# Optimization experiments

Measured on AMD Instinct MI355X. Metric: run time of the kernel, lower is better.

The kernel has to match this reference:

```python
import jax, jax.numpy as jnp
import numpy as np
from jax import lax

B, N = 4096, 512          # batch, sequence length (input_dim = 2*N)
H1, H2 = 64, 256          # hidden sizes of the two stacked LSTMs
E = 20                    # embed dim
OUT = 2


def _lstm_step(x, h, c, Wih, Whh, b):
    # gates in PyTorch order: i, f, g, o
    g = x @ Wih.T + h @ Whh.T + b
    i, f, gg, o = jnp.split(g, 4, axis=-1)
    c_new = jax.nn.sigmoid(f) * c + jax.nn.sigmoid(i) * jnp.tanh(gg)
    h_new = jax.nn.sigmoid(o) * jnp.tanh(c_new)
    return h_new, c_new


def setup_inputs() -> dict:
    key = jax.random.key(0)
    ks = jax.random.split(key, 9)
    s = lambda fan_in: 1.0 / np.sqrt(fan_in)
    return {
        "x": jax.random.normal(ks[0], (B, 2 * N), dtype=jnp.float32),
        "W_embed": jax.random.uniform(ks[1], (E, 2), minval=-s(2), maxval=s(2), dtype=jnp.float32),
        "Wih1": jax.random.uniform(ks[2], (4 * H1, E), minval=-s(H1), maxval=s(H1), dtype=jnp.float32),
        "Whh1": jax.random.uniform(ks[3], (4 * H1, H1), minval=-s(H1), maxval=s(H1), dtype=jnp.float32),
        "b1": jax.random.uniform(ks[4], (4 * H1,), minval=-s(H1), maxval=s(H1), dtype=jnp.float32),
        "Wih2": jax.random.uniform(ks[5], (4 * H2, H1), minval=-s(H2), maxval=s(H2), dtype=jnp.float32),
        "Whh2": jax.random.uniform(ks[6], (4 * H2, H2), minval=-s(H2), maxval=s(H2), dtype=jnp.float32),
        "b2": jax.random.uniform(ks[7], (4 * H2,), minval=-s(H2), maxval=s(H2), dtype=jnp.float32),
        "Wout": jax.random.uniform(ks[8], (OUT, H2), minval=-s(H2), maxval=s(H2), dtype=jnp.float32),
        "bout": jnp.zeros((OUT,), dtype=jnp.float32),
    }


def reference(x, W_embed, Wih1, Whh1, b1, Wih2, Whh2, b2, Wout, bout):
    b = x.shape[0]
    tokens = x.reshape(b, -1, 2).transpose(1, 0, 2)         # (n, b, 2)
    embedded = jax.nn.relu(tokens @ W_embed.T)              # (n, b, 20)

    def step(carry, xt):
        h, c = carry
        h, c = _lstm_step(xt, h, c, Wih1, Whh1, b1)
        return (h, c), None

    h0 = jnp.zeros((b, H1), dtype=x.dtype)
    (h64, _), _ = lax.scan(step, (h0, h0), embedded)        # last hidden (b, 64)

    # second LSTM applied to the 2-D last-hidden as a single timestep
    hz = jnp.zeros((b, H2), dtype=x.dtype)
    h256, _ = _lstm_step(h64, hz, hz, Wih2, Whh2, b2)       # (b, 256)

    return h256 @ Wout.T + bout                             # (b, 2)
```

## Files before the change

kernel.cpp:

```cpp
#include <hip/hip_runtime.h>

typedef _Float16 f16x8 __attribute__((ext_vector_type(8)));
typedef float    f32x4 __attribute__((ext_vector_type(4)));

#define NSTEP 512
#define CHUNK 8
#define NCHUNK (NSTEP / CHUNK)
#define LOG2E     1.4426950408889634f
#define TWOLOG2E  2.8853900817779268f

__device__ __forceinline__ float exp2_(float v) { return __builtin_amdgcn_exp2f(v); }

__device__ __forceinline__ float lstm_act_(float gi, float gf, float gg, float go, float& c) {
    float eg = exp2_(gg);
    float ei = exp2_(gi);
    float ef = exp2_(gf);
    float eo = exp2_(go);
    float X  = (eg + 1.0f) * (1.0f + ei);
    float Y  = 1.0f + ef;
    float r  = __builtin_amdgcn_rcpf(X * Y);
    c = fmaf(r * X, c, (eg - 1.0f) * (r * Y));
    float ec = exp2_(fminf(c * TWOLOG2E, 30.0f));
    float r2 = __builtin_amdgcn_rcpf((ec + 1.0f) * (1.0f + eo));
    return (ec - 1.0f) * r2;
}
__device__ __forceinline__ float sig_(float v) {
    return __builtin_amdgcn_rcpf(1.0f + exp2_(-v * LOG2E));
}
__device__ __forceinline__ float tanh_(float v) {
    return 1.0f - 2.0f * __builtin_amdgcn_rcpf(exp2_(v * TWOLOG2E) + 1.0f);
}

__device__ __forceinline__ void bar_() {
    asm volatile("s_waitcnt lgkmcnt(0)" ::: "memory");
    __builtin_amdgcn_s_barrier();
    asm volatile("" ::: "memory");
}

__global__ __launch_bounds__(512, 2) void lstm_mfma16_kernel(
    const float* __restrict__ x,     const float* __restrict__ Wemb,
    const float* __restrict__ Wih1,  const float* __restrict__ Whh1,
    const float* __restrict__ b1,    const float* __restrict__ Wih2,
    const float* __restrict__ b2,    const float* __restrict__ Wout,
    const float* __restrict__ bout,  float* __restrict__ out)
{
    __shared__ __align__(16) _Float16 P[2][2][4][16][8];
    __shared__ __align__(16) _Float16 Pe[2][CHUNK][4][16][8];
    __shared__ __align__(16) float h2tmp[16 * 64];
    __shared__ __align__(16) float h2s[256 * 16];
    __shared__ float part[32 * 16 * 2];

    const int t   = threadIdx.x;
    const int l   = t & 63;
    const int w   = t >> 6;
    const int m   = l & 15;
    const int q   = l >> 4;
    const int b0  = blockIdx.x * 16;

    f16x8 whh[2][2], whE[2];
    f32x4 bias4[2];
    #pragma unroll
    for (int tt = 0; tt < 2; ++tt) {
        const int tau = 2 * w + tt;
        const int g = m & 3;
        const float sc = (g == 2) ? TWOLOG2E : -LOG2E;
        const int n = g * 64 + 4 * tau + (m >> 2);
        #pragma unroll
        for (int c = 0; c < 2; ++c)
            #pragma unroll
            for (int jj = 0; jj < 8; ++jj)
                whh[tt][c][jj] = (_Float16)(Whh1[n * 64 + c * 32 + (q << 3) + jj] * sc);
        #pragma unroll
        for (int jj = 0; jj < 8; ++jj) {
            int k = (q << 3) + jj;
            whE[tt][jj] = (_Float16)((k < 20) ? Wih1[n * 20 + k] * sc : 0.0f);
        }
        #pragma unroll
        for (int r = 0; r < 4; ++r) {
            float scr = (r == 2) ? TWOLOG2E : -LOG2E;
            bias4[tt][r] = b1[r * 64 + 4 * tau + q] * scr;
        }
    }

    const int myuA = 8 * w + q;
    const int myuB = 8 * w + 4 + q;
    _Float16* hwA = &P[0][myuA >> 5][(myuA >> 3) & 3][m][myuA & 7];
    _Float16* hwB = &P[0][myuB >> 5][(myuB >> 3) & 3][m][myuB & 7];
    const _Float16* rb = &P[0][0][q][m][0];

    const float* xp[5]; _Float16* pe[5];
    float we0[5], we1[5];
    float2 xv[5];
    #pragma unroll
    for (int k = 0; k < 5; ++k) {
        int v  = t + 512 * k;
        int d  = v % 20, pr = v / 20;
        int bb = pr & 15, s = pr >> 4;
        we0[k] = Wemb[2 * d];
        we1[k] = Wemb[2 * d + 1];
        pe[k]  = &Pe[0][s][d >> 3][bb][d & 7];
        xp[k]  = x + (size_t)(b0 + bb) * (2 * NSTEP) + 2 * s;
        xv[k]  = *(const float2*)xp[k];
    }

    ((_Float16*)P)[t]       = (_Float16)0.0f;
    ((_Float16*)P)[t + 512] = (_Float16)0.0f;
    {
        _Float16* pz = (_Float16*)Pe;
        #pragma unroll
        for (int k = 0; k < 16; ++k) pz[t + 512 * k] = (_Float16)0.0f;
    }
    __syncthreads();
    #pragma unroll
    for (int k = 0; k < 5; ++k)
        pe[k][0] = (_Float16)fmaxf(fmaf(xv[k].x, we0[k], xv[k].y * we1[k]), 0.0f);
    #pragma unroll
    for (int k = 0; k < 5; ++k) { xp[k] += 16; xv[k] = *(const float2*)xp[k]; }
    __syncthreads();

    float cA = 0.0f, cB = 0.0f;
    for (int ch = 0; ch < NCHUNK; ++ch) {
        const int pb = ch & 1;
        const _Float16* peR = (const _Float16*)Pe + pb * 4096;

        f32x4 axA[CHUNK], axB[CHUNK];
        #pragma unroll
        for (int j = 0; j < CHUNK; ++j) {
            f16x8 fe = *(const f16x8*)(peR + j * 512 + q * 128 + m * 8);
            axA[j] = __builtin_amdgcn_mfma_f32_16x16x32_f16(whE[0], fe, bias4[0], 0, 0, 0);
            axB[j] = __builtin_amdgcn_mfma_f32_16x16x32_f16(whE[1], fe, bias4[1], 0, 0, 0);
        }

        #pragma unroll
        for (int j = 0; j < CHUNK; ++j) {
            const int pr = j & 1;
            f16x8 f0 = *(const f16x8*)(rb + pr * 1024);
            f16x8 f1 = *(const f16x8*)(rb + pr * 1024 + 512);
            f32x4 aA = __builtin_amdgcn_mfma_f32_16x16x32_f16(whh[0][0], f0, axA[j], 0, 0, 0);
            f32x4 aB = __builtin_amdgcn_mfma_f32_16x16x32_f16(whh[1][0], f0, axB[j], 0, 0, 0);
            aA = __builtin_amdgcn_mfma_f32_16x16x32_f16(whh[0][1], f1, aA, 0, 0, 0);
            aB = __builtin_amdgcn_mfma_f32_16x16x32_f16(whh[1][1], f1, aB, 0, 0, 0);
            float hA = lstm_act_(aA[0], aA[1], aA[2], aA[3], cA);
            float hB = lstm_act_(aB[0], aB[1], aB[2], aB[3], cB);
            hwA[(pr ^ 1) * 1024] = (_Float16)hA;
            hwB[(pr ^ 1) * 1024] = (_Float16)hB;
            if (j == 0) {
                #pragma unroll
                for (int k = 0; k < 5; ++k)
                    pe[k][(pb ^ 1) * 4096] =
                        (_Float16)fmaxf(fmaf(xv[k].x, we0[k], xv[k].y * we1[k]), 0.0f);
                if (ch + 2 < NCHUNK) {
                    #pragma unroll
                    for (int k = 0; k < 5; ++k) { xp[k] += 16; xv[k] = *(const float2*)xp[k]; }
                }
            }
            bar_();
        }
    }

    #pragma unroll
    for (int r = 0; r < 2; ++r) {
        int tt = t + 512 * r;
        int b = tt >> 6, k = tt & 63;
        h2tmp[tt] = (float)P[0][k >> 5][(k >> 3) & 3][b][k & 7];
    }
    __syncthreads();

    {
        const int u = t & 255;
        const int bh0 = (t >> 8) * 8;
        float acci[8], accg[8], acco[8];
        float bi2 = b2[u], bg2 = b2[512 + u], bo2 = b2[768 + u];
        #pragma unroll
        for (int b = 0; b < 8; ++b) { acci[b] = bi2; accg[b] = bg2; acco[b] = bo2; }
        for (int k4 = 0; k4 < 64; k4 += 4) {
            float4 wi = *(const float4*)&Wih2[(size_t)u * 64 + k4];
            float4 wg = *(const float4*)&Wih2[(size_t)(512 + u) * 64 + k4];
            float4 wo = *(const float4*)&Wih2[(size_t)(768 + u) * 64 + k4];
            #pragma unroll
            for (int b = 0; b < 8; ++b) {
                float4 hb = *(const float4*)&h2tmp[(bh0 + b) * 64 + k4];
                acci[b] += wi.x * hb.x + wi.y * hb.y + wi.z * hb.z + wi.w * hb.w;
                accg[b] += wg.x * hb.x + wg.y * hb.y + wg.z * hb.z + wg.w * hb.w;
                acco[b] += wo.x * hb.x + wo.y * hb.y + wo.z * hb.z + wo.w * hb.w;
            }
        }
        #pragma unroll
        for (int b = 0; b < 8; ++b) {
            float c2 = sig_(acci[b]) * tanh_(accg[b]);
            h2s[u * 16 + bh0 + b] = sig_(acco[b]) * tanh_(c2);
        }
    }
    __syncthreads();

    {
        int b = t & 15, grp = t >> 4;
        float p0 = 0.f, p1 = 0.f;
        #pragma unroll
        for (int uu = grp * 8; uu < grp * 8 + 8; ++uu) {
            float hvv = h2s[uu * 16 + b];
            p0 += hvv * Wout[uu];
            p1 += hvv * Wout[256 + uu];
        }
        part[(grp * 16 + b) * 2 + 0] = p0;
        part[(grp * 16 + b) * 2 + 1] = p1;
    }
    __syncthreads();
    if (t < 32) {
        int b = t >> 1, o = t & 1;
        float s0 = bout[o];
        for (int grp = 0; grp < 32; ++grp) s0 += part[(grp * 16 + b) * 2 + o];
        out[(size_t)(b0 + b) * 2 + o] = s0;
    }
}

extern "C" void kernel_launch(void* const* d_in, const int* in_sizes, int n_in,
                              void* d_out, int out_size, void* d_ws, size_t ws_size,
                              hipStream_t stream) {
    const float* x    = (const float*)d_in[0];
    const float* Wemb = (const float*)d_in[1];
    const float* Wih1 = (const float*)d_in[2];
    const float* Whh1 = (const float*)d_in[3];
    const float* b1   = (const float*)d_in[4];
    const float* Wih2 = (const float*)d_in[5];
    const float* b2   = (const float*)d_in[7];
    const float* Wout = (const float*)d_in[8];
    const float* bout = (const float*)d_in[9];
    float* out = (float*)d_out;

    lstm_mfma16_kernel<<<256, 512, 0, stream>>>(
        x, Wemb, Wih1, Whh1, b1, Wih2, b2, Wout, bout, out);
}
```

Before: 291.7 us.

## Halve block to four waves, each computing four gate tiles per step

Shrinks the workgroup from 512 to 256 threads. Each wave now owns four 16-unit gate tiles of the recurrent LSTM instead of two. The embedding chunk drops from 8 to 4 steps, and the second-LSTM and output tail are remapped to 16 batches per thread. The aim is to make the per-timestep barrier cheaper by syncing fewer waves and to give each wave more independent MFMA chains for ILP. The cost is one wave per SIMD, which leaves less cross-wave latency hiding, plus more registers per wave.

```diff
diff --git a/kernel.cpp b/kernel.cpp
--- a/kernel.cpp
+++ b/kernel.cpp
@@ -4,7 +4,7 @@
 typedef float    f32x4 __attribute__((ext_vector_type(4)));
 
 #define NSTEP 512
-#define CHUNK 8
+#define CHUNK 4
 #define NCHUNK (NSTEP / CHUNK)
 #define LOG2E     1.4426950408889634f
 #define TWOLOG2E  2.8853900817779268f
@@ -37,7 +37,7 @@
     asm volatile("" ::: "memory");
 }
 
-__global__ __launch_bounds__(512, 2) void lstm_mfma16_kernel(
+__global__ __launch_bounds__(256, 1) void lstm_mfma16_kernel(
     const float* __restrict__ x,     const float* __restrict__ Wemb,
     const float* __restrict__ Wih1,  const float* __restrict__ Whh1,
     const float* __restrict__ b1,    const float* __restrict__ Wih2,
@@ -48,7 +48,7 @@
     __shared__ __align__(16) _Float16 Pe[2][CHUNK][4][16][8];
     __shared__ __align__(16) float h2tmp[16 * 64];
     __shared__ __align__(16) float h2s[256 * 16];
-    __shared__ float part[32 * 16 * 2];
+    __shared__ float part[16 * 16 * 2];
 
     const int t   = threadIdx.x;
     const int l   = t & 63;
@@ -57,11 +57,11 @@
     const int q   = l >> 4;
     const int b0  = blockIdx.x * 16;
 
-    f16x8 whh[2][2], whE[2];
-    f32x4 bias4[2];
-    #pragma unroll
-    for (int tt = 0; tt < 2; ++tt) {
-        const int tau = 2 * w + tt;
+    f16x8 whh[4][2], whE[4];
+    f32x4 bias4[4];
+    #pragma unroll
+    for (int tt = 0; tt < 4; ++tt) {
+        const int tau = 4 * w + tt;
         const int g = m & 3;
         const float sc = (g == 2) ? TWOLOG2E : -LOG2E;
         const int n = g * 64 + 4 * tau + (m >> 2);
@@ -82,10 +82,12 @@
         }
     }
 
-    const int myuA = 8 * w + q;
-    const int myuB = 8 * w + 4 + q;
-    _Float16* hwA = &P[0][myuA >> 5][(myuA >> 3) & 3][m][myuA & 7];
-    _Float16* hwB = &P[0][myuB >> 5][(myuB >> 3) & 3][m][myuB & 7];
+    _Float16* hw[4];
+    #pragma unroll
+    for (int tt = 0; tt < 4; ++tt) {
+        const int myu = 16 * w + 4 * tt + q;
+        hw[tt] = &P[0][myu >> 5][(myu >> 3) & 3][m][myu & 7];
+    }
     const _Float16* rb = &P[0][0][q][m][0];
 
     const float* xp[5]; _Float16* pe[5];
@@ -93,7 +95,7 @@
     float2 xv[5];
     #pragma unroll
     for (int k = 0; k < 5; ++k) {
-        int v  = t + 512 * k;
+        int v  = t + 256 * k;
         int d  = v % 20, pr = v / 20;
         int bb = pr & 15, s = pr >> 4;
         we0[k] = Wemb[2 * d];
@@ -103,32 +105,33 @@
         xv[k]  = *(const float2*)xp[k];
     }
 
-    ((_Float16*)P)[t]       = (_Float16)0.0f;
-    ((_Float16*)P)[t + 512] = (_Float16)0.0f;
+    #pragma unroll
+    for (int k = 0; k < 8; ++k) ((_Float16*)P)[t + 256 * k] = (_Float16)0.0f;
     {
         _Float16* pz = (_Float16*)Pe;
         #pragma unroll
-        for (int k = 0; k < 16; ++k) pz[t + 512 * k] = (_Float16)0.0f;
+        for (int k = 0; k < 16; ++k) pz[t + 256 * k] = (_Float16)0.0f;
     }
     __syncthreads();
     #pragma unroll
     for (int k = 0; k < 5; ++k)
         pe[k][0] = (_Float16)fmaxf(fmaf(xv[k].x, we0[k], xv[k].y * we1[k]), 0.0f);
     #pragma unroll
-    for (int k = 0; k < 5; ++k) { xp[k] += 16; xv[k] = *(const float2*)xp[k]; }
-    __syncthreads();
-
-    float cA = 0.0f, cB = 0.0f;
+    for (int k = 0; k < 5; ++k) { xp[k] += 2 * CHUNK; xv[k] = *(const float2*)xp[k]; }
+    __syncthreads();
+
+    float cst[4] = {0.f, 0.f, 0.f, 0.f};
     for (int ch = 0; ch < NCHUNK; ++ch) {
         const int pb = ch & 1;
-        const _Float16* peR = (const _Float16*)Pe + pb * 4096;
-
-        f32x4 axA[CHUNK], axB[CHUNK];
+        const _Float16* peR = (const _Float16*)Pe + pb * 2048;
+
+        f32x4 ax[4][CHUNK];
         #pragma unroll
         for (int j = 0; j < CHUNK; ++j) {
             f16x8 fe = *(const f16x8*)(peR + j * 512 + q * 128 + m * 8);
-            axA[j] = __builtin_amdgcn_mfma_f32_16x16x32_f16(whE[0], fe, bias4[0], 0, 0, 0);
-            axB[j] = __builtin_amdgcn_mfma_f32_16x16x32_f16(whE[1], fe, bias4[1], 0, 0, 0);
+            #pragma unroll
+            for (int tt = 0; tt < 4; ++tt)
+                ax[tt][j] = __builtin_amdgcn_mfma_f32_16x16x32_f16(whE[tt], fe, bias4[tt], 0, 0, 0);
         }
 
         #pragma unroll
@@ -136,22 +139,26 @@
             const int pr = j & 1;
             f16x8 f0 = *(const f16x8*)(rb + pr * 1024);
             f16x8 f1 = *(const f16x8*)(rb + pr * 1024 + 512);
-            f32x4 aA = __builtin_amdgcn_mfma_f32_16x16x32_f16(whh[0][0], f0, axA[j], 0, 0, 0);
-            f32x4 aB = __builtin_amdgcn_mfma_f32_16x16x32_f16(whh[1][0], f0, axB[j], 0, 0, 0);
-            aA = __builtin_amdgcn_mfma_f32_16x16x32_f16(whh[0][1], f1, aA, 0, 0, 0);
-            aB = __builtin_amdgcn_mfma_f32_16x16x32_f16(whh[1][1], f1, aB, 0, 0, 0);
-            float hA = lstm_act_(aA[0], aA[1], aA[2], aA[3], cA);
-            float hB = lstm_act_(aB[0], aB[1], aB[2], aB[3], cB);
-            hwA[(pr ^ 1) * 1024] = (_Float16)hA;
-            hwB[(pr ^ 1) * 1024] = (_Float16)hB;
+            f32x4 a[4];
+            #pragma unroll
+            for (int tt = 0; tt < 4; ++tt)
+                a[tt] = __builtin_amdgcn_mfma_f32_16x16x32_f16(whh[tt][0], f0, ax[tt][j], 0, 0, 0);
+            #pragma unroll
+            for (int tt = 0; tt < 4; ++tt)
+                a[tt] = __builtin_amdgcn_mfma_f32_16x16x32_f16(whh[tt][1], f1, a[tt], 0, 0, 0);
+            #pragma unroll
+            for (int tt = 0; tt < 4; ++tt) {
+                float hv = lstm_act_(a[tt][0], a[tt][1], a[tt][2], a[tt][3], cst[tt]);
+                hw[tt][(pr ^ 1) * 1024] = (_Float16)hv;
+            }
             if (j == 0) {
                 #pragma unroll
                 for (int k = 0; k < 5; ++k)
-                    pe[k][(pb ^ 1) * 4096] =
+                    pe[k][(pb ^ 1) * 2048] =
                         (_Float16)fmaxf(fmaf(xv[k].x, we0[k], xv[k].y * we1[k]), 0.0f);
                 if (ch + 2 < NCHUNK) {
                     #pragma unroll
-                    for (int k = 0; k < 5; ++k) { xp[k] += 16; xv[k] = *(const float2*)xp[k]; }
+                    for (int k = 0; k < 5; ++k) { xp[k] += 2 * CHUNK; xv[k] = *(const float2*)xp[k]; }
                 }
             }
             bar_();
@@ -159,36 +166,35 @@
     }
 
     #pragma unroll
-    for (int r = 0; r < 2; ++r) {
-        int tt = t + 512 * r;
+    for (int r = 0; r < 4; ++r) {
+        int tt = t + 256 * r;
         int b = tt >> 6, k = tt & 63;
         h2tmp[tt] = (float)P[0][k >> 5][(k >> 3) & 3][b][k & 7];
     }
     __syncthreads();
 
     {
-        const int u = t & 255;
-        const int bh0 = (t >> 8) * 8;
-        float acci[8], accg[8], acco[8];
+        const int u = t;
+        float acci[16], accg[16], acco[16];
         float bi2 = b2[u], bg2 = b2[512 + u], bo2 = b2[768 + u];
         #pragma unroll
-        for (int b = 0; b < 8; ++b) { acci[b] = bi2; accg[b] = bg2; acco[b] = bo2; }
+        for (int b = 0; b < 16; ++b) { acci[b] = bi2; accg[b] = bg2; acco[b] = bo2; }
         for (int k4 = 0; k4 < 64; k4 += 4) {
             float4 wi = *(const float4*)&Wih2[(size_t)u * 64 + k4];
             float4 wg = *(const float4*)&Wih2[(size_t)(512 + u) * 64 + k4];
             float4 wo = *(const float4*)&Wih2[(size_t)(768 + u) * 64 + k4];
             #pragma unroll
-            for (int b = 0; b < 8; ++b) {
-                float4 hb = *(const float4*)&h2tmp[(bh0 + b) * 64 + k4];
+            for (int b = 0; b < 16; ++b) {
+                float4 hb = *(const float4*)&h2tmp[b * 64 + k4];
                 acci[b] += wi.x * hb.x + wi.y * hb.y + wi.z * hb.z + wi.w * hb.w;
                 accg[b] += wg.x * hb.x + wg.y * hb.y + wg.z * hb.z + wg.w * hb.w;
                 acco[b] += wo.x * hb.x + wo.y * hb.y + wo.z * hb.z + wo.w * hb.w;
             }
         }
         #pragma unroll
-        for (int b = 0; b < 8; ++b) {
+        for (int b = 0; b < 16; ++b) {
             float c2 = sig_(acci[b]) * tanh_(accg[b]);
-            h2s[u * 16 + bh0 + b] = sig_(acco[b]) * tanh_(c2);
+            h2s[u * 16 + b] = sig_(acco[b]) * tanh_(c2);
         }
     }
     __syncthreads();
@@ -197,7 +203,7 @@
         int b = t & 15, grp = t >> 4;
         float p0 = 0.f, p1 = 0.f;
         #pragma unroll
-        for (int uu = grp * 8; uu < grp * 8 + 8; ++uu) {
+        for (int uu = grp * 16; uu < grp * 16 + 16; ++uu) {
             float hvv = h2s[uu * 16 + b];
             p0 += hvv * Wout[uu];
             p1 += hvv * Wout[256 + uu];
@@ -209,7 +215,7 @@
     if (t < 32) {
         int b = t >> 1, o = t & 1;
         float s0 = bout[o];
-        for (int grp = 0; grp < 32; ++grp) s0 += part[(grp * 16 + b) * 2 + o];
+        for (int grp = 0; grp < 16; ++grp) s0 += part[(grp * 16 + b) * 2 + o];
         out[(size_t)(b0 + b) * 2 + o] = s0;
     }
 }
@@ -228,6 +234,6 @@
     const float* bout = (const float*)d_in[9];
     float* out = (float*)d_out;
 
-    lstm_mfma16_kernel<<<256, 512, 0, stream>>>(
+    lstm_mfma16_kernel<<<256, 256, 0, stream>>>(
         x, Wemb, Wih1, Whh1, b1, Wih2, b2, Wout, bout, out);
 }
```

Result: slower. 322.0 us (+10.4%).

## Split recurrent step into two half-barriers to overlap activation with MFMA

Applied to the files above, without the earlier changes.

Splits each LSTM timestep into two phases. Hidden units are reassigned so that the A half of the hidden state (units 0-31) and the B half (32-63) are written at separate barriers. The first K-half MFMA for the next step can start as soon as the A half is ready, while the B activation runs in between. Input-projection MFMAs for the next chunk are prefetched mid-chunk with the chunk size halved, and the embedding load work shrinks to three slots per thread. This doubles the barrier count per step in exchange for a shorter dependency chain per step, and it changes which buffer holds the final hidden state.

```diff
diff --git a/kernel.cpp b/kernel.cpp
--- a/kernel.cpp
+++ b/kernel.cpp
@@ -4,7 +4,7 @@
 typedef float    f32x4 __attribute__((ext_vector_type(4)));
 
 #define NSTEP 512
-#define CHUNK 8
+#define CHUNK 4
 #define NCHUNK (NSTEP / CHUNK)
 #define LOG2E     1.4426950408889634f
 #define TWOLOG2E  2.8853900817779268f
@@ -57,44 +57,49 @@
     const int q   = l >> 4;
     const int b0  = blockIdx.x * 16;
 
-    f16x8 whh[2][2], whE[2];
-    f32x4 bias4[2];
-    #pragma unroll
-    for (int tt = 0; tt < 2; ++tt) {
-        const int tau = 2 * w + tt;
+    f16x8 whhA[2], whhB[2], whEA, whEB;
+    f32x4 biasA, biasB;
+    {
         const int g = m & 3;
         const float sc = (g == 2) ? TWOLOG2E : -LOG2E;
-        const int n = g * 64 + 4 * tau + (m >> 2);
+        const int nA = g * 64 + 4 * w + (m >> 2);
+        const int nB = g * 64 + 4 * (8 + w) + (m >> 2);
         #pragma unroll
         for (int c = 0; c < 2; ++c)
             #pragma unroll
-            for (int jj = 0; jj < 8; ++jj)
-                whh[tt][c][jj] = (_Float16)(Whh1[n * 64 + c * 32 + (q << 3) + jj] * sc);
+            for (int jj = 0; jj < 8; ++jj) {
+                whhA[c][jj] = (_Float16)(Whh1[nA * 64 + c * 32 + (q << 3) + jj] * sc);
+                whhB[c][jj] = (_Float16)(Whh1[nB * 64 + c * 32 + (q << 3) + jj] * sc);
+            }
         #pragma unroll
         for (int jj = 0; jj < 8; ++jj) {
             int k = (q << 3) + jj;
-            whE[tt][jj] = (_Float16)((k < 20) ? Wih1[n * 20 + k] * sc : 0.0f);
+            whEA[jj] = (_Float16)((k < 20) ? Wih1[nA * 20 + k] * sc : 0.0f);
+            whEB[jj] = (_Float16)((k < 20) ? Wih1[nB * 20 + k] * sc : 0.0f);
         }
         #pragma unroll
         for (int r = 0; r < 4; ++r) {
             float scr = (r == 2) ? TWOLOG2E : -LOG2E;
-            bias4[tt][r] = b1[r * 64 + 4 * tau + q] * scr;
-        }
-    }
-
-    const int myuA = 8 * w + q;
-    const int myuB = 8 * w + 4 + q;
-    _Float16* hwA = &P[0][myuA >> 5][(myuA >> 3) & 3][m][myuA & 7];
-    _Float16* hwB = &P[0][myuB >> 5][(myuB >> 3) & 3][m][myuB & 7];
+            biasA[r] = b1[r * 64 + 4 * w + q] * scr;
+            biasB[r] = b1[r * 64 + 4 * (8 + w) + q] * scr;
+        }
+    }
+
+    const int us = 4 * w + q;
+    _Float16* hwA = &P[0][0][us >> 3][m][us & 7];
+    _Float16* hwB = hwA + 512;
     const _Float16* rb = &P[0][0][q][m][0];
 
-    const float* xp[5]; _Float16* pe[5];
-    float we0[5], we1[5];
-    float2 xv[5];
-    #pragma unroll
-    for (int k = 0; k < 5; ++k) {
+    const float* xp[3]; _Float16* pe[3];
+    float we0[3], we1[3];
+    bool val[3];
+    float2 xv[3];
+    #pragma unroll
+    for (int k = 0; k < 3; ++k) {
         int v  = t + 512 * k;
-        int d  = v % 20, pr = v / 20;
+        val[k] = (v < CHUNK * 320);
+        int vv = val[k] ? v : 0;
+        int d  = vv % 20, pr = vv / 20;
         int bb = pr & 15, s = pr >> 4;
         we0[k] = Wemb[2 * d];
         we1[k] = Wemb[2 * d + 1];
@@ -103,58 +108,84 @@
         xv[k]  = *(const float2*)xp[k];
     }
 
-    ((_Float16*)P)[t]       = (_Float16)0.0f;
-    ((_Float16*)P)[t + 512] = (_Float16)0.0f;
-    {
-        _Float16* pz = (_Float16*)Pe;
-        #pragma unroll
-        for (int k = 0; k < 16; ++k) pz[t + 512 * k] = (_Float16)0.0f;
-    }
-    __syncthreads();
-    #pragma unroll
-    for (int k = 0; k < 5; ++k)
-        pe[k][0] = (_Float16)fmaxf(fmaf(xv[k].x, we0[k], xv[k].y * we1[k]), 0.0f);
-    #pragma unroll
-    for (int k = 0; k < 5; ++k) { xp[k] += 16; xv[k] = *(const float2*)xp[k]; }
-    __syncthreads();
+    #pragma unroll
+    for (int k = 0; k < 4; ++k) ((_Float16*)P)[t + 512 * k] = (_Float16)0.0f;
+    #pragma unroll
+    for (int k = 0; k < 8; ++k) ((_Float16*)Pe)[t + 512 * k] = (_Float16)0.0f;
+    __syncthreads();
+    #pragma unroll
+    for (int k = 0; k < 3; ++k)
+        if (val[k])
+            pe[k][0] = (_Float16)fmaxf(fmaf(xv[k].x, we0[k], xv[k].y * we1[k]), 0.0f);
+    #pragma unroll
+    for (int k = 0; k < 3; ++k) { xp[k] += 2 * CHUNK; xv[k] = *(const float2*)xp[k]; }
+    __syncthreads();
+
+    f32x4 xA0[CHUNK], xB0[CHUNK], xA1[CHUNK], xB1[CHUNK];
+    #pragma unroll
+    for (int j = 0; j < CHUNK; ++j) {
+        f16x8 fe = *(const f16x8*)((const _Float16*)Pe + j * 512 + q * 128 + m * 8);
+        xA0[j] = __builtin_amdgcn_mfma_f32_16x16x32_f16(whEA, fe, biasA, 0, 0, 0);
+        xB0[j] = __builtin_amdgcn_mfma_f32_16x16x32_f16(whEB, fe, biasB, 0, 0, 0);
+    }
+    f32x4 aA = xA0[0], aB = xB0[0];
 
     float cA = 0.0f, cB = 0.0f;
-    for (int ch = 0; ch < NCHUNK; ++ch) {
-        const int pb = ch & 1;
-        const _Float16* peR = (const _Float16*)Pe + pb * 4096;
-
-        f32x4 axA[CHUNK], axB[CHUNK];
-        #pragma unroll
-        for (int j = 0; j < CHUNK; ++j) {
-            f16x8 fe = *(const f16x8*)(peR + j * 512 + q * 128 + m * 8);
-            axA[j] = __builtin_amdgcn_mfma_f32_16x16x32_f16(whE[0], fe, bias4[0], 0, 0, 0);
-            axB[j] = __builtin_amdgcn_mfma_f32_16x16x32_f16(whE[1], fe, bias4[1], 0, 0, 0);
-        }
-
-        #pragma unroll
-        for (int j = 0; j < CHUNK; ++j) {
-            const int pr = j & 1;
-            f16x8 f0 = *(const f16x8*)(rb + pr * 1024);
-            f16x8 f1 = *(const f16x8*)(rb + pr * 1024 + 512);
-            f32x4 aA = __builtin_amdgcn_mfma_f32_16x16x32_f16(whh[0][0], f0, axA[j], 0, 0, 0);
-            f32x4 aB = __builtin_amdgcn_mfma_f32_16x16x32_f16(whh[1][0], f0, axB[j], 0, 0, 0);
-            aA = __builtin_amdgcn_mfma_f32_16x16x32_f16(whh[0][1], f1, aA, 0, 0, 0);
-            aB = __builtin_amdgcn_mfma_f32_16x16x32_f16(whh[1][1], f1, aB, 0, 0, 0);
-            float hA = lstm_act_(aA[0], aA[1], aA[2], aA[3], cA);
-            float hB = lstm_act_(aB[0], aB[1], aB[2], aB[3], cB);
-            hwA[(pr ^ 1) * 1024] = (_Float16)hA;
-            hwB[(pr ^ 1) * 1024] = (_Float16)hB;
-            if (j == 0) {
-                #pragma unroll
-                for (int k = 0; k < 5; ++k)
-                    pe[k][(pb ^ 1) * 4096] =
-                        (_Float16)fmaxf(fmaf(xv[k].x, we0[k], xv[k].y * we1[k]), 0.0f);
-                if (ch + 2 < NCHUNK) {
+    for (int chp = 0; chp < NCHUNK / 2; ++chp) {
+        #pragma unroll
+        for (int cb = 0; cb < 2; ++cb) {
+            const int ch = chp * 2 + cb;
+            #pragma unroll
+            for (int j = 0; j < CHUNK; ++j) {
+                const int wp = j & 1;
+                float hA = lstm_act_(aA[0], aA[1], aA[2], aA[3], cA);
+                hwA[wp * 1024] = (_Float16)hA;
+                bar_();
+                f16x8 f0 = *(const f16x8*)(rb + wp * 1024);
+                f32x4 pA, pB;
+                if (j < CHUNK - 1) {
+                    pA = __builtin_amdgcn_mfma_f32_16x16x32_f16(
+                        whhA[0], f0, cb == 0 ? xA0[j + 1] : xA1[j + 1], 0, 0, 0);
+                    pB = __builtin_amdgcn_mfma_f32_16x16x32_f16(
+                        whhB[0], f0, cb == 0 ? xB0[j + 1] : xB1[j + 1], 0, 0, 0);
+                } else {
+                    pA = __builtin_amdgcn_mfma_f32_16x16x32_f16(
+                        whhA[0], f0, cb == 0 ? xA1[0] : xA0[0], 0, 0, 0);
+                    pB = __builtin_amdgcn_mfma_f32_16x16x32_f16(
+                        whhB[0], f0, cb == 0 ? xB1[0] : xB0[0], 0, 0, 0);
+                }
+                if (j == 0) {
                     #pragma unroll
-                    for (int k = 0; k < 5; ++k) { xp[k] += 16; xv[k] = *(const float2*)xp[k]; }
+                    for (int k = 0; k < 3; ++k)
+                        if (val[k])
+                            pe[k][(cb ^ 1) * 2048] =
+                                (_Float16)fmaxf(fmaf(xv[k].x, we0[k], xv[k].y * we1[k]), 0.0f);
+                    if (ch + 2 < NCHUNK) {
+                        #pragma unroll
+                        for (int k = 0; k < 3; ++k) { xp[k] += 2 * CHUNK; xv[k] = *(const float2*)xp[k]; }
+                    }
                 }
+                if (j == 2) {
+                    const _Float16* peN = (const _Float16*)Pe + (cb ^ 1) * 2048;
+                    #pragma unroll
+                    for (int j2 = 0; j2 < CHUNK; ++j2) {
+                        f16x8 fe = *(const f16x8*)(peN + j2 * 512 + q * 128 + m * 8);
+                        if (cb == 0) {
+                            xA1[j2] = __builtin_amdgcn_mfma_f32_16x16x32_f16(whEA, fe, biasA, 0, 0, 0);
+                            xB1[j2] = __builtin_amdgcn_mfma_f32_16x16x32_f16(whEB, fe, biasB, 0, 0, 0);
+                        } else {
+                            xA0[j2] = __builtin_amdgcn_mfma_f32_16x16x32_f16(whEA, fe, biasA, 0, 0, 0);
+                            xB0[j2] = __builtin_amdgcn_mfma_f32_16x16x32_f16(whEB, fe, biasB, 0, 0, 0);
+                        }
+                    }
+                }
+                float hB = lstm_act_(aB[0], aB[1], aB[2], aB[3], cB);
+                hwB[wp * 1024] = (_Float16)hB;
+                bar_();
+                f16x8 f1 = *(const f16x8*)(rb + wp * 1024 + 512);
+                aA = __builtin_amdgcn_mfma_f32_16x16x32_f16(whhA[1], f1, pA, 0, 0, 0);
+                aB = __builtin_amdgcn_mfma_f32_16x16x32_f16(whhB[1], f1, pB, 0, 0, 0);
             }
-            bar_();
         }
     }
 
@@ -162,7 +193,7 @@
     for (int r = 0; r < 2; ++r) {
         int tt = t + 512 * r;
         int b = tt >> 6, k = tt & 63;
-        h2tmp[tt] = (float)P[0][k >> 5][(k >> 3) & 3][b][k & 7];
+        h2tmp[tt] = (float)P[1][k >> 5][(k >> 3) & 3][b][k & 7];
     }
     __syncthreads();
 
```

Result: slower. 354.1 us (+21.4%).

## Software-pipeline input projection one step ahead and split recurrent MFMA chains

Applied to the files above, without the earlier changes.

The input-projection MFMAs are now computed one timestep ahead inside the recurrent loop instead of being batched per chunk, which cuts register pressure from the per-chunk accumulator arrays. The two K-halves of the recurrent matmul now accumulate independently (the second from zero) and are summed before the activation, which shortens the dependent MFMA chain on the critical path. The chunk loop is unrolled by two so the double-buffer index is a compile-time constant. In exchange it adds extra VALU adds per step and one extra embedding read at the chunk boundary.

```diff
diff --git a/kernel.cpp b/kernel.cpp
--- a/kernel.cpp
+++ b/kernel.cpp
@@ -81,12 +81,14 @@
             bias4[tt][r] = b1[r * 64 + 4 * tau + q] * scr;
         }
     }
+    const f32x4 z4 = {0.f, 0.f, 0.f, 0.f};
 
     const int myuA = 8 * w + q;
     const int myuB = 8 * w + 4 + q;
     _Float16* hwA = &P[0][myuA >> 5][(myuA >> 3) & 3][m][myuA & 7];
     _Float16* hwB = &P[0][myuB >> 5][(myuB >> 3) & 3][m][myuB & 7];
     const _Float16* rb = &P[0][0][q][m][0];
+    const _Float16* base_pe = (const _Float16*)Pe + q * 128 + m * 8;
 
     const float* xp[5]; _Float16* pe[5];
     float we0[5], we1[5];
@@ -105,6 +107,8 @@
 
     ((_Float16*)P)[t]       = (_Float16)0.0f;
     ((_Float16*)P)[t + 512] = (_Float16)0.0f;
+    ((_Float16*)P)[t + 1024] = (_Float16)0.0f;
+    ((_Float16*)P)[t + 1536] = (_Float16)0.0f;
     {
         _Float16* pz = (_Float16*)Pe;
         #pragma unroll
@@ -115,46 +119,54 @@
     for (int k = 0; k < 5; ++k)
         pe[k][0] = (_Float16)fmaxf(fmaf(xv[k].x, we0[k], xv[k].y * we1[k]), 0.0f);
     #pragma unroll
-    for (int k = 0; k < 5; ++k) { xp[k] += 16; xv[k] = *(const float2*)xp[k]; }
-    __syncthreads();
+    for (int k = 0; k < 5; ++k) { xp[k] += 2 * CHUNK; xv[k] = *(const float2*)xp[k]; }
+    __syncthreads();
+
+    f32x4 axA, axB;
+    {
+        f16x8 fe0 = *(const f16x8*)(base_pe);
+        axA = __builtin_amdgcn_mfma_f32_16x16x32_f16(whE[0], fe0, bias4[0], 0, 0, 0);
+        axB = __builtin_amdgcn_mfma_f32_16x16x32_f16(whE[1], fe0, bias4[1], 0, 0, 0);
+    }
 
     float cA = 0.0f, cB = 0.0f;
-    for (int ch = 0; ch < NCHUNK; ++ch) {
-        const int pb = ch & 1;
-        const _Float16* peR = (const _Float16*)Pe + pb * 4096;
-
-        f32x4 axA[CHUNK], axB[CHUNK];
-        #pragma unroll
-        for (int j = 0; j < CHUNK; ++j) {
-            f16x8 fe = *(const f16x8*)(peR + j * 512 + q * 128 + m * 8);
-            axA[j] = __builtin_amdgcn_mfma_f32_16x16x32_f16(whE[0], fe, bias4[0], 0, 0, 0);
-            axB[j] = __builtin_amdgcn_mfma_f32_16x16x32_f16(whE[1], fe, bias4[1], 0, 0, 0);
-        }
-
-        #pragma unroll
-        for (int j = 0; j < CHUNK; ++j) {
-            const int pr = j & 1;
-            f16x8 f0 = *(const f16x8*)(rb + pr * 1024);
-            f16x8 f1 = *(const f16x8*)(rb + pr * 1024 + 512);
-            f32x4 aA = __builtin_amdgcn_mfma_f32_16x16x32_f16(whh[0][0], f0, axA[j], 0, 0, 0);
-            f32x4 aB = __builtin_amdgcn_mfma_f32_16x16x32_f16(whh[1][0], f0, axB[j], 0, 0, 0);
-            aA = __builtin_amdgcn_mfma_f32_16x16x32_f16(whh[0][1], f1, aA, 0, 0, 0);
-            aB = __builtin_amdgcn_mfma_f32_16x16x32_f16(whh[1][1], f1, aB, 0, 0, 0);
-            float hA = lstm_act_(aA[0], aA[1], aA[2], aA[3], cA);
-            float hB = lstm_act_(aB[0], aB[1], aB[2], aB[3], cB);
-            hwA[(pr ^ 1) * 1024] = (_Float16)hA;
-            hwB[(pr ^ 1) * 1024] = (_Float16)hB;
-            if (j == 0) {
-                #pragma unroll
-                for (int k = 0; k < 5; ++k)
-                    pe[k][(pb ^ 1) * 4096] =
-                        (_Float16)fmaxf(fmaf(xv[k].x, we0[k], xv[k].y * we1[k]), 0.0f);
-                if (ch + 2 < NCHUNK) {
+    for (int chp = 0; chp < NCHUNK / 2; ++chp) {
+        #pragma unroll
+        for (int cb = 0; cb < 2; ++cb) {
+            const int ch = 2 * chp + cb;
+            #pragma unroll
+            for (int j = 0; j < CHUNK; ++j) {
+                const int pr = j & 1;
+                f16x8 f0 = *(const f16x8*)(rb + pr * 1024);
+                f16x8 f1 = *(const f16x8*)(rb + pr * 1024 + 512);
+                const int nxt = (j < CHUNK - 1) ? (cb * 4096 + (j + 1) * 512)
+                                                : ((cb ^ 1) * 4096);
+                f16x8 feN = *(const f16x8*)(base_pe + nxt);
+                f32x4 nA = __builtin_amdgcn_mfma_f32_16x16x32_f16(whE[0], feN, bias4[0], 0, 0, 0);
+                f32x4 nB = __builtin_amdgcn_mfma_f32_16x16x32_f16(whE[1], feN, bias4[1], 0, 0, 0);
+                f32x4 aA0 = __builtin_amdgcn_mfma_f32_16x16x32_f16(whh[0][0], f0, axA, 0, 0, 0);
+                f32x4 aB0 = __builtin_amdgcn_mfma_f32_16x16x32_f16(whh[1][0], f0, axB, 0, 0, 0);
+                f32x4 aA1 = __builtin_amdgcn_mfma_f32_16x16x32_f16(whh[0][1], f1, z4, 0, 0, 0);
+                f32x4 aB1 = __builtin_amdgcn_mfma_f32_16x16x32_f16(whh[1][1], f1, z4, 0, 0, 0);
+                float hA = lstm_act_(aA0[0] + aA1[0], aA0[1] + aA1[1],
+                                     aA0[2] + aA1[2], aA0[3] + aA1[3], cA);
+                hwA[(pr ^ 1) * 1024] = (_Float16)hA;
+                float hB = lstm_act_(aB0[0] + aB1[0], aB0[1] + aB1[1],
+                                     aB0[2] + aB1[2], aB0[3] + aB1[3], cB);
+                hwB[(pr ^ 1) * 1024] = (_Float16)hB;
+                if (j == 0) {
                     #pragma unroll
-                    for (int k = 0; k < 5; ++k) { xp[k] += 16; xv[k] = *(const float2*)xp[k]; }
+                    for (int k = 0; k < 5; ++k)
+                        pe[k][(cb ^ 1) * 4096] =
+                            (_Float16)fmaxf(fmaf(xv[k].x, we0[k], xv[k].y * we1[k]), 0.0f);
+                    if (ch + 2 < NCHUNK) {
+                        #pragma unroll
+                        for (int k = 0; k < 5; ++k) { xp[k] += 2 * CHUNK; xv[k] = *(const float2*)xp[k]; }
+                    }
                 }
+                axA = nA; axB = nB;
+                bar_();
             }
-            bar_();
         }
     }
 
```

Result: slower. 314.9 us (+8.0%).
